# Optimization experiments

Measured on AMD Instinct MI355X. Metric: run time of the kernel, lower is better.

The kernel has to match this reference:

```python
import jax, jax.numpy as jnp
import numpy as np

N = 100_000   # nodes
E = 6_400_000  # edges (avg degree 64)
K = 3          # TAGConv hops -> K+1 linear terms per layer


def setup_inputs() -> dict:
    key = jax.random.key(0)
    ks = jax.random.split(key, 9)
    return {
        "x": jax.random.normal(ks[0], (N,), jnp.float32),
        "edge_index": jax.random.randint(ks[1], (2, E), 0, N, jnp.int32),
        "edge_attr": jax.random.normal(ks[2], (E,), jnp.float32),
        "k": 5000,
        "W1": jax.random.normal(ks[3], (K + 1, 1, 8), jnp.float32) * 0.5,
        "b1": jax.random.normal(ks[4], (8,), jnp.float32) * 0.1,
        "W2": jax.random.normal(ks[5], (K + 1, 8, 8), jnp.float32) * 0.2,
        "b2": jax.random.normal(ks[6], (8,), jnp.float32) * 0.1,
        "W3": jax.random.normal(ks[7], (K + 1, 8, 1), jnp.float32) * 0.2,
        "b3": jax.random.normal(ks[8], (1,), jnp.float32) * 0.1,
    }


def _gcn_norm(src, dst, edge_weight, num_nodes):
    # PyG gcn_norm with add_self_loops=False: deg over target index,
    # norm_e = d^{-1/2}[src] * w_e * d^{-1/2}[dst]
    deg = jax.ops.segment_sum(edge_weight, dst, num_segments=num_nodes)
    dis = jnp.where(deg > 0, jax.lax.rsqrt(jnp.where(deg > 0, deg, 1.0)), 0.0)
    return dis[src] * edge_weight * dis[dst]


def _tagconv(x, W, b, src, dst, norm, num_nodes):
    # out = sum_{h=0..K} (A_norm^h x) @ W[h] + b
    out = x @ W[0]
    h = x
    for i in range(1, W.shape[0]):
        h = jax.ops.segment_sum(norm[:, None] * h[src], dst, num_segments=num_nodes)
        out = out + h @ W[i]
    return out + b


def reference(x, edge_index, edge_attr, k, W1, b1, W2, b2, W3, b3):
    num_nodes = x.shape[0]
    x = x[:, None]  # [N, 1]
    src, dst = edge_index[0], edge_index[1]
    norm = _gcn_norm(src, dst, jnp.abs(edge_attr), num_nodes)

    x = jax.nn.relu(_tagconv(x, W1, b1, src, dst, norm, num_nodes))
    x = jax.nn.relu(_tagconv(x, W2, b2, src, dst, norm, num_nodes))
    x = jax.nn.relu(_tagconv(x, W3, b3, src, dst, norm, num_nodes))

    # tg.nn.InstanceNorm(1), batch=None, affine=False: normalize over all nodes
    mean = jnp.mean(x)
    var = jnp.mean((x - mean) ** 2)
    x = ((x - mean) * jax.lax.rsqrt(var + 1e-5)).squeeze(-1)  # [N]

    # top-k one-hot mask (argsort descending -> first k indices)
    _, top_idx = jax.lax.top_k(x, k)
    top_vec = jnp.zeros_like(x).at[top_idx].set(1.0)
    return jnp.column_stack((x, top_vec))  # [N, 2]
```

## Files before the change

kernel.cpp:

```cpp
#include <hip/hip_runtime.h>

#define BS 256
#define GPN 16
#define NBLKB 1024
#define BSH 8
#define SMAX 400

static __device__ __forceinline__ float relu_(float v) { return fmaxf(v, 0.0f); }


__global__ void k_binhist(const int* __restrict__ dst, int* __restrict__ bcnt,
                          int E, int chunk, int nbuck) {
  __shared__ int h[1024];
  int b = blockIdx.x, t = threadIdx.x;
  for (int i = t; i < nbuck; i += BS) h[i] = 0;
  __syncthreads();
  int beg = b * chunk, end = min(E, beg + chunk);
  for (int e = beg + t; e < end; e += BS) atomicAdd(&h[dst[e] >> BSH], 1);
  __syncthreads();
  for (int i = t; i < nbuck; i += BS) bcnt[(size_t)i * NBLKB + b] = h[i];
}

__global__ void k_bucketscan(int* __restrict__ bcnt, int* __restrict__ btot) {
  __shared__ int sh[BS];
  int bkt = blockIdx.x, t = threadIdx.x;
  size_t base = (size_t)bkt * NBLKB;
  int c[4], s = 0;
#pragma unroll
  for (int j = 0; j < 4; ++j) { c[j] = bcnt[base + t * 4 + j]; s += c[j]; }
  sh[t] = s; __syncthreads();
  for (int off = 1; off < BS; off <<= 1) {
    int add = (t >= off) ? sh[t - off] : 0; __syncthreads();
    sh[t] += add; __syncthreads();
  }
  int run = sh[t] - s;
#pragma unroll
  for (int j = 0; j < 4; ++j) { bcnt[base + t * 4 + j] = run; run += c[j]; }
  if (t == BS - 1) btot[bkt] = run;
}

__global__ void k_basescan(const int* __restrict__ btot, int* __restrict__ bbase, int nbuck) {
  __shared__ int sh[BS];
  int t = threadIdx.x;
  int run = 0;
  for (int c = 0; c < nbuck; c += BS) {
    int i = c + t;
    int v = (i < nbuck) ? btot[i] : 0;
    sh[t] = v; __syncthreads();
    for (int off = 1; off < BS; off <<= 1) {
      int add = (t >= off) ? sh[t - off] : 0; __syncthreads();
      sh[t] += add; __syncthreads();
    }
    if (i < nbuck) bbase[i] = run + sh[t] - v;
    run += sh[BS - 1];
    __syncthreads();
  }
}

__global__ void k_bin(const int* __restrict__ src, const int* __restrict__ dst,
                      const float* __restrict__ attr, const int* __restrict__ bcnt,
                      const int* __restrict__ bbase, int2* __restrict__ bed,
                      int E, int chunk, int nbuck) {
  __shared__ int2 stage[SMAX][8];
  __shared__ int  fc[SMAX];
  __shared__ int  cur[SMAX];
  int b = blockIdx.x, t = threadIdx.x;
  for (int i = t; i < nbuck; i += BS) {
    cur[i] = bbase[i] + bcnt[(size_t)i * NBLKB + b];
    fc[i] = 0;
  }
  __syncthreads();
  int beg = b * chunk, end = min(E, beg + chunk);
  for (int base = beg; base < end; base += BS) {
    int e = base + t;
    if (e < end) {
      int d = dst[e];
      int bkt = d >> BSH;
      int2 rec = make_int2((int)(((unsigned)(d & ((1 << BSH) - 1)) << 17) | (unsigned)src[e]),
                           __float_as_int(fabsf(attr[e])));
      int slot = atomicAdd(&fc[bkt], 1);
      if (slot < 8) stage[bkt][slot] = rec;
      else { int gp = atomicAdd(&cur[bkt], 1); bed[gp] = rec; }
    }
    __syncthreads();
    for (int i = t; i < nbuck; i += BS) {
      int c = fc[i]; if (c > 8) c = 8;
      if (c == 8) {
        int gp = cur[i]; cur[i] = gp + 8;
#pragma unroll
        for (int j = 0; j < 8; ++j) bed[gp + j] = stage[i][j];
        fc[i] = 0;
      }
    }
    __syncthreads();
  }
  for (int i = t; i < nbuck; i += BS) {
    int c = fc[i]; if (c > 8) c = 8;
    if (c) {
      int gp = cur[i];
      for (int j = 0; j < c; ++j) bed[gp + j] = stage[i][j];
    }
  }
}

__global__ void k_cntdeg(const int2* __restrict__ bed, const int* __restrict__ bbase,
                         const int* __restrict__ btot, const float* __restrict__ x,
                         float* __restrict__ dis, float* __restrict__ xhat,
                         int* __restrict__ rowptr, int N, int E) {
  __shared__ int   lc[1 << BSH];
  __shared__ float ld[1 << BSH];
  __shared__ int   sc[1 << BSH];
  int bkt = blockIdx.x, t = threadIdx.x;
  lc[t] = 0; ld[t] = 0.f;
  __syncthreads();
  int beg = bbase[bkt], tot = btot[bkt];
  for (int i = t; i < tot; i += BS) {
    int2 rec = bed[beg + i];
    int dl = (int)((unsigned)rec.x >> 17);
    atomicAdd(&lc[dl], 1);
    atomicAdd(&ld[dl], __int_as_float(rec.y));
  }
  __syncthreads();
  int c = lc[t];
  sc[t] = c;
  __syncthreads();
  for (int off = 1; off < BS; off <<= 1) {
    int add = (t >= off) ? sc[t - off] : 0; __syncthreads();
    sc[t] += add; __syncthreads();
  }
  int n = (bkt << BSH) + t;
  if (n < N) {
    rowptr[n] = beg + sc[t] - c;
    float dg = ld[t];
    float d = (dg > 0.f) ? (1.0f / sqrtf(dg)) : 0.f;
    dis[n] = d;
    xhat[n] = d * x[n];
  }
  if (t == 0 && bkt == (int)gridDim.x - 1) rowptr[N] = E;
}

__global__ void k_fill(const int2* __restrict__ bed, const int* __restrict__ bbase,
                       const int* __restrict__ btot, const int* __restrict__ rowptr,
                       int2* __restrict__ adj, int N) {
  __shared__ int2 stage[1 << BSH][8];
  __shared__ int  fc[1 << BSH];
  __shared__ int  rcur[1 << BSH];
  int bkt = blockIdx.x, t = threadIdx.x;
  int n = (bkt << BSH) + t;
  rcur[t] = (n < N) ? rowptr[n] : 0;
  fc[t] = 0;
  __syncthreads();
  int beg = bbase[bkt], tot = btot[bkt];
  for (int base = 0; base < tot; base += BS) {
    int i = base + t;
    if (i < tot) {
      int2 rec = bed[beg + i];
      unsigned u = (unsigned)rec.x;
      int dl = (int)(u >> 17);
      int2 orec = make_int2((int)(u & 0x1FFFFu), rec.y);
      int slot = atomicAdd(&fc[dl], 1);
      if (slot < 8) stage[dl][slot] = orec;
      else { int gp = atomicAdd(&rcur[dl], 1); adj[gp] = orec; }
    }
    __syncthreads();
    {
      int c = fc[t]; if (c > 8) c = 8;
      if (c == 8) {
        int gp = rcur[t]; rcur[t] = gp + 8;
#pragma unroll
        for (int j = 0; j < 8; ++j) adj[gp + j] = stage[t][j];
        fc[t] = 0;
      }
    }
    __syncthreads();
  }
  {
    int c = fc[t]; if (c > 8) c = 8;
    if (c) {
      int gp = rcur[t];
      for (int j = 0; j < c; ++j) adj[gp + j] = stage[t][j];
    }
  }
}


__global__ void k_scanA(const int* __restrict__ cnt, int* __restrict__ bsum, int N) {
  __shared__ int sh[BS];
  int t = threadIdx.x;
  int base = blockIdx.x * 1024;
  int s = 0;
#pragma unroll
  for (int j = 0; j < 4; ++j) { int i = base + t * 4 + j; s += (i < N) ? cnt[i] : 0; }
  sh[t] = s; __syncthreads();
  for (int off = 128; off; off >>= 1) { if (t < off) sh[t] += sh[t + off]; __syncthreads(); }
  if (t == 0) bsum[blockIdx.x] = sh[0];
}

__global__ void k_scanB(int* __restrict__ bsum, int NB2) {
  __shared__ int sh[BS];
  int t = threadIdx.x;
  int v = (t < NB2) ? bsum[t] : 0;
  sh[t] = v; __syncthreads();
  for (int off = 1; off < BS; off <<= 1) {
    int add = (t >= off) ? sh[t - off] : 0; __syncthreads();
    sh[t] += add; __syncthreads();
  }
  if (t < NB2) bsum[t] = sh[t] - v;
}

__global__ void k_scanC(const int* __restrict__ cnt, const int* __restrict__ bsum,
                        int* __restrict__ rowptr, int* __restrict__ cursor, int N, int E) {
  __shared__ int sh[BS];
  int b = blockIdx.x, t = threadIdx.x;
  int base = b * 1024;
  int c[4]; int s = 0;
#pragma unroll
  for (int j = 0; j < 4; ++j) { int i = base + t * 4 + j; c[j] = (i < N) ? cnt[i] : 0; s += c[j]; }
  sh[t] = s; __syncthreads();
  for (int off = 1; off < BS; off <<= 1) {
    int add = (t >= off) ? sh[t - off] : 0; __syncthreads();
    sh[t] += add; __syncthreads();
  }
  int run = sh[t] - s + bsum[b];
#pragma unroll
  for (int j = 0; j < 4; ++j) {
    int i = base + t * 4 + j;
    if (i < N) { rowptr[i] = run; if (cursor) cursor[i] = run; run += c[j]; }
  }
  if (b == 0 && t == 0) rowptr[N] = E;
}


__global__ void k_count(const int* __restrict__ dst, int* __restrict__ cnt, int E) {
  int e = blockIdx.x * blockDim.x + threadIdx.x;
  if (e < E) atomicAdd(&cnt[dst[e]], 1);
}

__global__ void k_place(const int* __restrict__ src, const int* __restrict__ dst,
                        const float* __restrict__ attr, int* __restrict__ cursor,
                        int2* __restrict__ adj, int E) {
  int e = blockIdx.x * blockDim.x + threadIdx.x;
  if (e >= E) return;
  int d = dst[e];
  int pos = atomicAdd(&cursor[d], 1);
  adj[pos] = make_int2(src[e], __float_as_int(fabsf(attr[e])));
}

__global__ void k_degdis(const int* __restrict__ rowptr, const int2* __restrict__ adj,
                         const float* __restrict__ x, float* __restrict__ dis,
                         float* __restrict__ xhat, int N) {
  int g = (blockIdx.x * blockDim.x + threadIdx.x) / GPN;
  int l = threadIdx.x & (GPN - 1);
  if (g >= N) return;
  int beg = rowptr[g], end = rowptr[g + 1];
  float s = 0.0f;
  for (int e = beg + l; e < end; e += GPN) s += __int_as_float(adj[e].y);
#pragma unroll
  for (int off = 8; off; off >>= 1) s += __shfl_xor(s, off, GPN);
  if (l == 0) {
    float d = (s > 0.0f) ? (1.0f / sqrtf(s)) : 0.0f;
    dis[g] = d;
    xhat[g] = d * x[g];
  }
}


__global__ void k_gp1_uh(const int* __restrict__ rowptr, const int2* __restrict__ adj,
                         const float* __restrict__ uin, const float* __restrict__ dis,
                         float* __restrict__ hout, float* __restrict__ uout, int N) {
  int g = (blockIdx.x * blockDim.x + threadIdx.x) / GPN;
  int l = threadIdx.x & (GPN - 1);
  if (g >= N) return;
  int beg = rowptr[g], end = rowptr[g + 1];
  float acc = 0.0f;
  for (int e = beg + l; e < end; e += GPN) {
    int2 sw = adj[e];
    acc += __int_as_float(sw.y) * uin[sw.x];
  }
#pragma unroll
  for (int off = 8; off; off >>= 1) acc += __shfl_xor(acc, off, GPN);
  if (l == 0) {
    float d = dis[g];
    float h = d * acc;
    hout[g] = h;
    uout[g] = d * h;
  }
}

__global__ void k_gp1_y(const int* __restrict__ rowptr, const int2* __restrict__ adj,
                        const float* __restrict__ u2, const float* __restrict__ x,
                        const float* __restrict__ h1, const float* __restrict__ h2,
                        const float* __restrict__ dis, const float* __restrict__ W1,
                        const float* __restrict__ b1, const float* __restrict__ W23,
                        float* __restrict__ y, float* __restrict__ Phat, int N) {
  int g = (blockIdx.x * blockDim.x + threadIdx.x) / GPN;
  int l = threadIdx.x & (GPN - 1);
  if (g >= N) return;
  int beg = rowptr[g], end = rowptr[g + 1];
  float acc = 0.0f;
  for (int e = beg + l; e < end; e += GPN) {
    int2 sw = adj[e];
    acc += __int_as_float(sw.y) * u2[sw.x];
  }
#pragma unroll
  for (int off = 8; off; off >>= 1) acc += __shfl_xor(acc, off, GPN);
  if (l == 0) {
    float d = dis[g];
    float xv = x[g], a = h1[g], b = h2[g], c = d * acc;
    float o[8];
#pragma unroll
    for (int j = 0; j < 8; ++j)
      o[j] = relu_(xv * W1[j] + a * W1[8 + j] + b * W1[16 + j] + c * W1[24 + j] + b1[j]);
    float4* op = (float4*)(y + (size_t)g * 8);
    op[0] = make_float4(o[0], o[1], o[2], o[3]);
    op[1] = make_float4(o[4], o[5], o[6], o[7]);
    float p[8];
#pragma unroll
    for (int j = 0; j < 8; ++j) {
      float s = 0.0f;
#pragma unroll
      for (int i = 0; i < 8; ++i) s += o[i] * W23[i * 8 + j];
      p[j] = d * s;
    }
    float4* pp = (float4*)(Phat + (size_t)g * 8);
    pp[0] = make_float4(p[0], p[1], p[2], p[3]);
    pp[1] = make_float4(p[4], p[5], p[6], p[7]);
  }
}

__global__ void k_gp8_u(const int* __restrict__ rowptr, const int2* __restrict__ adj,
                        const float* __restrict__ uin, const float* __restrict__ y,
                        const float* __restrict__ W, const float* __restrict__ dis,
                        float* __restrict__ uout, int N) {
  int g = (blockIdx.x * blockDim.x + threadIdx.x) / GPN;
  int l = threadIdx.x & (GPN - 1);
  if (g >= N) return;
  int beg = rowptr[g], end = rowptr[g + 1];
  float a0=0,a1=0,a2=0,a3=0,a4=0,a5=0,a6=0,a7=0;
  for (int e = beg + l; e < end; e += GPN) {
    int2 sw = adj[e];
    float w = __int_as_float(sw.y);
    const float4* hp = (const float4*)(uin + (size_t)sw.x * 8);
    float4 u = hp[0], v = hp[1];
    a0 += w*u.x; a1 += w*u.y; a2 += w*u.z; a3 += w*u.w;
    a4 += w*v.x; a5 += w*v.y; a6 += w*v.z; a7 += w*v.w;
  }
#pragma unroll
  for (int off = 8; off; off >>= 1) {
    a0 += __shfl_xor(a0, off, GPN); a1 += __shfl_xor(a1, off, GPN);
    a2 += __shfl_xor(a2, off, GPN); a3 += __shfl_xor(a3, off, GPN);
    a4 += __shfl_xor(a4, off, GPN); a5 += __shfl_xor(a5, off, GPN);
    a6 += __shfl_xor(a6, off, GPN); a7 += __shfl_xor(a7, off, GPN);
  }
  if (l == 0) {
    float d = dis[g];
    const float4* yp = (const float4*)(y + (size_t)g * 8);
    float4 u = yp[0], v = yp[1];
    float yi[8] = {u.x, u.y, u.z, u.w, v.x, v.y, v.z, v.w};
    float acc[8] = {a0, a1, a2, a3, a4, a5, a6, a7};
    float o[8];
#pragma unroll
    for (int j = 0; j < 8; ++j) {
      float s = 0.0f;
#pragma unroll
      for (int i = 0; i < 8; ++i) s += yi[i] * W[i * 8 + j];
      o[j] = d * (s + d * acc[j]);
    }
    float4* op = (float4*)(uout + (size_t)g * 8);
    op[0] = make_float4(o[0], o[1], o[2], o[3]);
    op[1] = make_float4(o[4], o[5], o[6], o[7]);
  }
}

__global__ void k_gp8_fin(const int* __restrict__ rowptr, const int2* __restrict__ adj,
                          const float* __restrict__ uin, const float* __restrict__ y,
                          const float* __restrict__ W0, const float* __restrict__ b2,
                          const float* __restrict__ W3, const float* __restrict__ dis,
                          float* __restrict__ S3hat, float* __restrict__ B2,
                          float* __restrict__ B1, float* __restrict__ B0, int N) {
  int g = (blockIdx.x * blockDim.x + threadIdx.x) / GPN;
  int l = threadIdx.x & (GPN - 1);
  if (g >= N) return;
  int beg = rowptr[g], end = rowptr[g + 1];
  float a0=0,a1=0,a2=0,a3=0,a4=0,a5=0,a6=0,a7=0;
  for (int e = beg + l; e < end; e += GPN) {
    int2 sw = adj[e];
    float w = __int_as_float(sw.y);
    const float4* hp = (const float4*)(uin + (size_t)sw.x * 8);
    float4 u = hp[0], v = hp[1];
    a0 += w*u.x; a1 += w*u.y; a2 += w*u.z; a3 += w*u.w;
    a4 += w*v.x; a5 += w*v.y; a6 += w*v.z; a7 += w*v.w;
  }
#pragma unroll
  for (int off = 8; off; off >>= 1) {
    a0 += __shfl_xor(a0, off, GPN); a1 += __shfl_xor(a1, off, GPN);
    a2 += __shfl_xor(a2, off, GPN); a3 += __shfl_xor(a3, off, GPN);
    a4 += __shfl_xor(a4, off, GPN); a5 += __shfl_xor(a5, off, GPN);
    a6 += __shfl_xor(a6, off, GPN); a7 += __shfl_xor(a7, off, GPN);
  }
  if (l == 0) {
    float d = dis[g];
    const float4* yp = (const float4*)(y + (size_t)g * 8);
    float4 u = yp[0], v = yp[1];
    float yi[8] = {u.x, u.y, u.z, u.w, v.x, v.y, v.z, v.w};
    float acc[8] = {a0, a1, a2, a3, a4, a5, a6, a7};
    float z[8];
#pragma unroll
    for (int j = 0; j < 8; ++j) {
      float s = 0.0f;
#pragma unroll
      for (int i = 0; i < 8; ++i) s += yi[i] * W0[i * 8 + j];
      z[j] = relu_(s + d * acc[j] + b2[j]);
    }
    float t[4];
#pragma unroll
    for (int i = 0; i < 4; ++i) {
      float s = 0.0f;
#pragma unroll
      for (int j = 0; j < 8; ++j) s += z[j] * W3[i * 8 + j];
      t[i] = s;
    }
    B0[g] = t[0]; B1[g] = t[1]; B2[g] = t[2];
    S3hat[g] = d * t[3];
  }
}

__global__ void k_gp1_bu(const int* __restrict__ rowptr, const int2* __restrict__ adj,
                         const float* __restrict__ uin, const float* __restrict__ B,
                         const float* __restrict__ dis, float* __restrict__ uout, int N) {
  int g = (blockIdx.x * blockDim.x + threadIdx.x) / GPN;
  int l = threadIdx.x & (GPN - 1);
  if (g >= N) return;
  int beg = rowptr[g], end = rowptr[g + 1];
  float acc = 0.0f;
  for (int e = beg + l; e < end; e += GPN) {
    int2 sw = adj[e];
    acc += __int_as_float(sw.y) * uin[sw.x];
  }
#pragma unroll
  for (int off = 8; off; off >>= 1) acc += __shfl_xor(acc, off, GPN);
  if (l == 0) {
    float d = dis[g];
    uout[g] = d * (B[g] + d * acc);
  }
}

__global__ void k_gp1_last(const int* __restrict__ rowptr, const int2* __restrict__ adj,
                           const float* __restrict__ uin, const float* __restrict__ B0,
                           const float* __restrict__ b3, const float* __restrict__ dis,
                           float* __restrict__ r, unsigned* __restrict__ keys,
                           double* __restrict__ partials, int N) {
  __shared__ double s1[BS];
  __shared__ double s2[BS];
  int tid = blockIdx.x * blockDim.x + threadIdx.x;
  int g = tid / GPN, l = tid & (GPN - 1);
  float rv = 0.0f;
  bool writer = false;
  if (g < N) {
    int beg = rowptr[g], end = rowptr[g + 1];
    float acc = 0.0f;
    for (int e = beg + l; e < end; e += GPN) {
      int2 sw = adj[e];
      acc += __int_as_float(sw.y) * uin[sw.x];
    }
#pragma unroll
    for (int off = 8; off; off >>= 1) acc += __shfl_xor(acc, off, GPN);
    if (l == 0) {
      float gg = B0[g] + dis[g] * acc;
      rv = relu_(gg + b3[0]);
      r[g] = rv;
      keys[g] = __float_as_uint(rv) | 0x80000000u;
      writer = true;
    }
  }
  double v = writer ? (double)rv : 0.0;
  s1[threadIdx.x] = v;
  s2[threadIdx.x] = v * v;
  __syncthreads();
  for (int off = 128; off; off >>= 1) {
    if (threadIdx.x < off) {
      s1[threadIdx.x] += s1[threadIdx.x + off];
      s2[threadIdx.x] += s2[threadIdx.x + off];
    }
    __syncthreads();
  }
  if (threadIdx.x == 0) {
    partials[2 * (size_t)blockIdx.x]     = s1[0];
    partials[2 * (size_t)blockIdx.x + 1] = s2[0];
  }
}

__global__ void k_stats(const double* __restrict__ partials, int nparts,
                        float* __restrict__ stats, int N) {
  __shared__ double s1[BS];
  __shared__ double s2[BS];
  int t = threadIdx.x;
  double a = 0.0, b = 0.0;
  for (int i = t; i < nparts; i += BS) { a += partials[2 * (size_t)i]; b += partials[2 * (size_t)i + 1]; }
  s1[t] = a; s2[t] = b;
  __syncthreads();
  for (int off = 128; off; off >>= 1) {
    if (t < off) { s1[t] += s1[t + off]; s2[t] += s2[t + off]; }
    __syncthreads();
  }
  if (t == 0) {
    double mean = s1[0] / (double)N;
    double var  = s2[0] / (double)N - mean * mean;
    stats[0] = (float)mean;
    stats[1] = (float)(1.0 / sqrt(var + 1e-5));
  }
}


__global__ void k_stateinit(unsigned* __restrict__ state, const int* __restrict__ kp) {
  state[0] = 0u;
  state[1] = (unsigned)kp[0];
}

__global__ void k_hist(const unsigned* __restrict__ keys, int N,
                       const unsigned* __restrict__ state, unsigned* __restrict__ hist,
                       int shift) {
  __shared__ unsigned sh[256];
  sh[threadIdx.x] = 0;
  __syncthreads();
  unsigned prefix = state[0];
  unsigned hmask = (shift >= 24) ? 0u : (0xFFFFFFFFu << (shift + 8));
  int stride = gridDim.x * blockDim.x;
  for (int n = blockIdx.x * blockDim.x + threadIdx.x; n < N; n += stride) {
    unsigned kk = keys[n];
    if ((kk & hmask) == (prefix & hmask)) atomicAdd(&sh[(kk >> shift) & 255u], 1u);
  }
  __syncthreads();
  atomicAdd(&hist[threadIdx.x], sh[threadIdx.x]);
}

__global__ void k_select(unsigned* __restrict__ state, unsigned* __restrict__ hist, int shift) {
  __shared__ unsigned sh[BS];
  int t = threadIdx.x;
  unsigned c = hist[t];
  sh[t] = c;
  __syncthreads();
  for (int off = 1; off < BS; off <<= 1) {
    unsigned add = (t + off < BS) ? sh[t + off] : 0u; __syncthreads();
    sh[t] += add; __syncthreads();
  }
  unsigned rem = state[1];
  unsigned S = sh[t];
  if (S >= rem && (S - c) < rem) {
    state[0] |= ((unsigned)t) << shift;
    state[1] = rem - (S - c);
  }
  hist[t] = 0;
}

__global__ void k_mark(const unsigned* __restrict__ keys, const float* __restrict__ r,
                       const float* __restrict__ stats, int N,
                       const unsigned* __restrict__ state, float* __restrict__ out,
                       unsigned* __restrict__ blkcnt) {
  unsigned T = state[0];
  float mean = stats[0], istd = stats[1];
  int n = blockIdx.x * 256 + threadIdx.x;
  int eq = 0;
  __shared__ int sh;
  if (threadIdx.x == 0) sh = 0;
  __syncthreads();
  if (n < N) {
    out[2 * (size_t)n] = (r[n] - mean) * istd;
    unsigned kk = keys[n];
    out[2 * (size_t)n + 1] = (kk > T) ? 1.0f : 0.0f;
    eq = (kk == T);
  }
  if (eq) atomicAdd(&sh, 1);
  __syncthreads();
  if (threadIdx.x == 0) blkcnt[blockIdx.x] = (unsigned)sh;
}

__global__ void k_scanP(const unsigned* __restrict__ blkcnt, unsigned* __restrict__ scanbuf, int NB) {
  __shared__ unsigned sh[BS];
  int t = threadIdx.x;
  unsigned c0 = (2 * t < NB) ? blkcnt[2 * t] : 0u;
  unsigned c1 = (2 * t + 1 < NB) ? blkcnt[2 * t + 1] : 0u;
  unsigned s = c0 + c1;
  sh[t] = s; __syncthreads();
  for (int off = 1; off < BS; off <<= 1) {
    unsigned add = (t >= off) ? sh[t - off] : 0u; __syncthreads();
    sh[t] += add; __syncthreads();
  }
  unsigned ex = sh[t] - s;
  if (2 * t < NB) scanbuf[2 * t] = ex;
  if (2 * t + 1 < NB) scanbuf[2 * t + 1] = ex + c0;
}

__global__ void k_resolve(const unsigned* __restrict__ keys, int N,
                          const unsigned* __restrict__ state,
                          const unsigned* __restrict__ scanbuf, float* __restrict__ out) {
  unsigned T = state[0];
  unsigned m = state[1];
  int n = blockIdx.x * 256 + threadIdx.x;
  if (n >= N) return;
  if (keys[n] != T) return;
  unsigned rank = scanbuf[blockIdx.x];
  int base = blockIdx.x * 256;
  for (int j = base; j < n; ++j) rank += (keys[j] == T);
  out[2 * (size_t)n + 1] = (rank < m) ? 1.0f : 0.0f;
}


extern "C" void kernel_launch(void* const* d_in, const int* in_sizes, int n_in,
                              void* d_out, int out_size, void* d_ws, size_t ws_size,
                              hipStream_t stream) {
  const float* x    = (const float*)d_in[0];
  const int*   ei   = (const int*)d_in[1];
  const float* attr = (const float*)d_in[2];
  const int*   kp   = (const int*)d_in[3];
  const float* W1   = (const float*)d_in[4];
  const float* b1   = (const float*)d_in[5];
  const float* W2   = (const float*)d_in[6];
  const float* b2   = (const float*)d_in[7];
  const float* W3   = (const float*)d_in[8];
  const float* b3   = (const float*)d_in[9];
  const int N = in_sizes[0];
  const int E = in_sizes[2];
  const int* src = ei;
  const int* dst = ei + E;
  float* out = (float*)d_out;
  const int NB    = (N + 255) / 256;
  const int NB2   = (N + 1023) / 1024;
  const int NBUCK = (N + (1 << BSH) - 1) >> BSH;
  const int chunk = (E + NBLKB - 1) / NBLKB;
  const int GGB   = (int)(((size_t)N * GPN + BS - 1) / BS);

  char* p = (char*)d_ws;
  auto alloc = [&](size_t bytes) -> char* {
    char* r = p; p += (bytes + 255) & ~(size_t)255; return r;
  };
  float*    dis    = (float*)alloc((size_t)N * 4);
  float*    xhat   = (float*)alloc((size_t)N * 4);
  float*    h1     = (float*)alloc((size_t)N * 4);
  float*    h2     = (float*)alloc((size_t)N * 4);
  float*    u1     = (float*)alloc((size_t)N * 4);
  float*    u2     = (float*)alloc((size_t)N * 4);
  float*    y      = (float*)alloc((size_t)N * 32);
  float*    Phat   = (float*)alloc((size_t)N * 32);
  float*    Qhat   = (float*)alloc((size_t)N * 32);
  float*    S3hat  = (float*)alloc((size_t)N * 4);
  float*    B2     = (float*)alloc((size_t)N * 4);
  float*    B1     = (float*)alloc((size_t)N * 4);
  float*    B0     = (float*)alloc((size_t)N * 4);
  float*    g2hat  = (float*)alloc((size_t)N * 4);
  float*    g1hat  = (float*)alloc((size_t)N * 4);
  float*    r      = (float*)alloc((size_t)N * 4);
  unsigned* keys   = (unsigned*)alloc((size_t)N * 4);
  double*   parts  = (double*)alloc((size_t)GGB * 16);
  float*    stats  = (float*)alloc(8);
  unsigned* state  = (unsigned*)alloc(8);
  unsigned* hist   = (unsigned*)alloc(1024);
  unsigned* blkcnt = (unsigned*)alloc((size_t)NB * 4);
  unsigned* scanbf = (unsigned*)alloc((size_t)NB * 4);
  int*      rowptr = (int*)alloc((size_t)(N + 1) * 4);
  int*      cursor = (int*)alloc((size_t)N * 4);
  int*      cnt    = (int*)alloc((size_t)N * 4);
  int*      bsum   = (int*)alloc(2048);
  int2*     adj    = (int2*)alloc((size_t)E * 8);
  size_t need_mid = (size_t)(p - (char*)d_ws);
  int2*     bed    = (int2*)alloc((size_t)E * 8);
  int*      bcnt   = (int*)alloc((size_t)NBUCK * NBLKB * 4);
  int*      btot   = (int*)alloc((size_t)NBUCK * 4 + 256);
  int*      bbase  = (int*)alloc((size_t)NBUCK * 4 + 256);
  size_t need_new = (size_t)(p - (char*)d_ws);

  dim3 B(BS);
  int genb = (E + BS - 1) / BS;
  dim3 GE(genb), GG(GGB), GN(NB), GB(NBUCK);

  bool use_new = (need_new <= ws_size) && (N <= 131072) && (NBUCK <= SMAX);

  hipMemsetAsync(hist, 0, 1024, stream);

  if (use_new) {
    k_binhist<<<dim3(NBLKB), B, 0, stream>>>(dst, bcnt, E, chunk, NBUCK);
    k_bucketscan<<<GB, B, 0, stream>>>(bcnt, btot);
    k_basescan<<<dim3(1), B, 0, stream>>>(btot, bbase, NBUCK);
    k_bin<<<dim3(NBLKB), B, 0, stream>>>(src, dst, attr, bcnt, bbase, bed, E, chunk, NBUCK);
    k_cntdeg<<<GB, B, 0, stream>>>(bed, bbase, btot, x, dis, xhat, rowptr, N, E);
    k_fill<<<GB, B, 0, stream>>>(bed, bbase, btot, rowptr, adj, N);
  } else {
    hipMemsetAsync(cnt, 0, (size_t)N * 4, stream);
    k_count<<<GE, B, 0, stream>>>(dst, cnt, E);
    k_scanA<<<dim3(NB2), B, 0, stream>>>(cnt, bsum, N);
    k_scanB<<<dim3(1), B, 0, stream>>>(bsum, NB2);
    k_scanC<<<dim3(NB2), B, 0, stream>>>(cnt, bsum, rowptr, cursor, N, E);
    k_place<<<GE, B, 0, stream>>>(src, dst, attr, cursor, adj, E);
    k_degdis<<<GG, B, 0, stream>>>(rowptr, adj, x, dis, xhat, N);
  }

  k_gp1_uh<<<GG, B, 0, stream>>>(rowptr, adj, xhat, dis, h1, u1, N);
  k_gp1_uh<<<GG, B, 0, stream>>>(rowptr, adj, u1, dis, h2, u2, N);
  k_gp1_y<<<GG, B, 0, stream>>>(rowptr, adj, u2, x, h1, h2, dis, W1, b1, W2 + 3 * 64, y, Phat, N);

  k_gp8_u<<<GG, B, 0, stream>>>(rowptr, adj, Phat, y, W2 + 2 * 64, dis, Qhat, N);
  k_gp8_u<<<GG, B, 0, stream>>>(rowptr, adj, Qhat, y, W2 + 1 * 64, dis, Phat, N);
  k_gp8_fin<<<GG, B, 0, stream>>>(rowptr, adj, Phat, y, W2, b2, W3, dis, S3hat, B2, B1, B0, N);

  k_gp1_bu<<<GG, B, 0, stream>>>(rowptr, adj, S3hat, B2, dis, g2hat, N);
  k_gp1_bu<<<GG, B, 0, stream>>>(rowptr, adj, g2hat, B1, dis, g1hat, N);
  k_gp1_last<<<GG, B, 0, stream>>>(rowptr, adj, g1hat, B0, b3, dis, r, keys, parts, N);

  k_stats<<<dim3(1), B, 0, stream>>>(parts, GGB, stats, N);

  k_stateinit<<<dim3(1), dim3(1), 0, stream>>>(state, kp);
  for (int shift = 24; shift >= 0; shift -= 8) {
    k_hist<<<GN, B, 0, stream>>>(keys, N, state, hist, shift);
    k_select<<<dim3(1), B, 0, stream>>>(state, hist, shift);
  }
  k_mark<<<GN, B, 0, stream>>>(keys, r, stats, N, state, out, blkcnt);
  k_scanP<<<dim3(1), B, 0, stream>>>(blkcnt, scanbf, NB);
  k_resolve<<<GN, B, 0, stream>>>(keys, N, state, scanbf, out);
}
```

Measured before the change: 581.9 us.

## Fuse CSR count/fill, widen binning blocks, unroll edge loops, single-block top-k select

Four separate changes. First, the degree-count and adjacency-fill kernels are merged into one 1024-thread kernel per bucket, with 16-slot staging per row. Second, the binning kernels move to 512-thread blocks, and the gather loops now use two independent accumulators per lane to expose more memory-level parallelism. Third, the four radix hist/select launch pairs are replaced by a single one-block kernel that runs all passes itself, removing launches and the global histogram memset. The cost is that this one block must serially scan all keys four times with only 256 threads.

```diff
diff --git a/kernel.cpp b/kernel.cpp
--- a/kernel.cpp
+++ b/kernel.cpp
@@ -1,6 +1,8 @@
 #include <hip/hip_runtime.h>
 
 #define BS 256
+#define BSB 512
+#define BSF 1024
 #define GPN 16
 #define NBLKB 1024
 #define BSH 8
@@ -13,12 +15,12 @@
                           int E, int chunk, int nbuck) {
   __shared__ int h[1024];
   int b = blockIdx.x, t = threadIdx.x;
-  for (int i = t; i < nbuck; i += BS) h[i] = 0;
+  for (int i = t; i < nbuck; i += BSB) h[i] = 0;
   __syncthreads();
   int beg = b * chunk, end = min(E, beg + chunk);
-  for (int e = beg + t; e < end; e += BS) atomicAdd(&h[dst[e] >> BSH], 1);
-  __syncthreads();
-  for (int i = t; i < nbuck; i += BS) bcnt[(size_t)i * NBLKB + b] = h[i];
+  for (int e = beg + t; e < end; e += BSB) atomicAdd(&h[dst[e] >> BSH], 1);
+  __syncthreads();
+  for (int i = t; i < nbuck; i += BSB) bcnt[(size_t)i * NBLKB + b] = h[i];
 }
 
 __global__ void k_bucketscan(int* __restrict__ bcnt, int* __restrict__ btot) {
@@ -65,13 +67,13 @@
   __shared__ int  fc[SMAX];
   __shared__ int  cur[SMAX];
   int b = blockIdx.x, t = threadIdx.x;
-  for (int i = t; i < nbuck; i += BS) {
+  for (int i = t; i < nbuck; i += BSB) {
     cur[i] = bbase[i] + bcnt[(size_t)i * NBLKB + b];
     fc[i] = 0;
   }
   __syncthreads();
   int beg = b * chunk, end = min(E, beg + chunk);
-  for (int base = beg; base < end; base += BS) {
+  for (int base = beg; base < end; base += BSB) {
     int e = base + t;
     if (e < end) {
       int d = dst[e];
@@ -83,7 +85,7 @@
       else { int gp = atomicAdd(&cur[bkt], 1); bed[gp] = rec; }
     }
     __syncthreads();
-    for (int i = t; i < nbuck; i += BS) {
+    for (int i = t; i < nbuck; i += BSB) {
       int c = fc[i]; if (c > 8) c = 8;
       if (c == 8) {
         int gp = cur[i]; cur[i] = gp + 8;
@@ -94,7 +96,7 @@
     }
     __syncthreads();
   }
-  for (int i = t; i < nbuck; i += BS) {
+  for (int i = t; i < nbuck; i += BSB) {
     int c = fc[i]; if (c > 8) c = 8;
     if (c) {
       int gp = cur[i];
@@ -103,55 +105,52 @@
   }
 }
 
-__global__ void k_cntdeg(const int2* __restrict__ bed, const int* __restrict__ bbase,
-                         const int* __restrict__ btot, const float* __restrict__ x,
-                         float* __restrict__ dis, float* __restrict__ xhat,
-                         int* __restrict__ rowptr, int N, int E) {
+__global__ void k_cntfill(const int2* __restrict__ bed, const int* __restrict__ bbase,
+                          const int* __restrict__ btot, const float* __restrict__ x,
+                          float* __restrict__ dis, float* __restrict__ xhat,
+                          int* __restrict__ rowptr, int2* __restrict__ adj, int N, int E) {
+  __shared__ int2  stage[1 << BSH][16];
   __shared__ int   lc[1 << BSH];
   __shared__ float ld[1 << BSH];
   __shared__ int   sc[1 << BSH];
+  __shared__ int   fc[1 << BSH];
+  __shared__ int   rcur[1 << BSH];
   int bkt = blockIdx.x, t = threadIdx.x;
-  lc[t] = 0; ld[t] = 0.f;
+  if (t < (1 << BSH)) { lc[t] = 0; ld[t] = 0.f; }
   __syncthreads();
   int beg = bbase[bkt], tot = btot[bkt];
-  for (int i = t; i < tot; i += BS) {
+  for (int i = t; i < tot; i += BSF) {
     int2 rec = bed[beg + i];
     int dl = (int)((unsigned)rec.x >> 17);
     atomicAdd(&lc[dl], 1);
     atomicAdd(&ld[dl], __int_as_float(rec.y));
   }
   __syncthreads();
-  int c = lc[t];
-  sc[t] = c;
-  __syncthreads();
-  for (int off = 1; off < BS; off <<= 1) {
-    int add = (t >= off) ? sc[t - off] : 0; __syncthreads();
-    sc[t] += add; __syncthreads();
-  }
-  int n = (bkt << BSH) + t;
-  if (n < N) {
-    rowptr[n] = beg + sc[t] - c;
-    float dg = ld[t];
-    float d = (dg > 0.f) ? (1.0f / sqrtf(dg)) : 0.f;
-    dis[n] = d;
-    xhat[n] = d * x[n];
-  }
-  if (t == 0 && bkt == (int)gridDim.x - 1) rowptr[N] = E;
-}
-
-__global__ void k_fill(const int2* __restrict__ bed, const int* __restrict__ bbase,
-                       const int* __restrict__ btot, const int* __restrict__ rowptr,
-                       int2* __restrict__ adj, int N) {
-  __shared__ int2 stage[1 << BSH][8];
-  __shared__ int  fc[1 << BSH];
-  __shared__ int  rcur[1 << BSH];
-  int bkt = blockIdx.x, t = threadIdx.x;
-  int n = (bkt << BSH) + t;
-  rcur[t] = (n < N) ? rowptr[n] : 0;
-  fc[t] = 0;
-  __syncthreads();
-  int beg = bbase[bkt], tot = btot[bkt];
-  for (int base = 0; base < tot; base += BS) {
+  if (t < (1 << BSH)) sc[t] = lc[t];
+  __syncthreads();
+  for (int off = 1; off < (1 << BSH); off <<= 1) {
+    int add = 0;
+    if (t < (1 << BSH) && t >= off) add = sc[t - off];
+    __syncthreads();
+    if (t < (1 << BSH)) sc[t] += add;
+    __syncthreads();
+  }
+  if (t < (1 << BSH)) {
+    int myrow = beg + sc[t] - lc[t];
+    rcur[t] = myrow;
+    fc[t] = 0;
+    int n = (bkt << BSH) + t;
+    if (n < N) {
+      rowptr[n] = myrow;
+      float dg = ld[t];
+      float d = (dg > 0.f) ? (1.0f / sqrtf(dg)) : 0.f;
+      dis[n] = d;
+      xhat[n] = d * x[n];
+    }
+  }
+  if (bkt == (int)gridDim.x - 1 && t == 0) rowptr[N] = E;
+  __syncthreads();
+  for (int base = 0; base < tot; base += BSF) {
     int i = base + t;
     if (i < tot) {
       int2 rec = bed[beg + i];
@@ -159,23 +158,23 @@
       int dl = (int)(u >> 17);
       int2 orec = make_int2((int)(u & 0x1FFFFu), rec.y);
       int slot = atomicAdd(&fc[dl], 1);
-      if (slot < 8) stage[dl][slot] = orec;
+      if (slot < 16) stage[dl][slot] = orec;
       else { int gp = atomicAdd(&rcur[dl], 1); adj[gp] = orec; }
     }
     __syncthreads();
-    {
-      int c = fc[t]; if (c > 8) c = 8;
-      if (c == 8) {
-        int gp = rcur[t]; rcur[t] = gp + 8;
-#pragma unroll
-        for (int j = 0; j < 8; ++j) adj[gp + j] = stage[t][j];
+    if (t < (1 << BSH)) {
+      int c = fc[t]; if (c > 16) c = 16;
+      if (c == 16) {
+        int gp = rcur[t]; rcur[t] = gp + 16;
+#pragma unroll
+        for (int j = 0; j < 16; ++j) adj[gp + j] = stage[t][j];
         fc[t] = 0;
       }
     }
     __syncthreads();
   }
-  {
-    int c = fc[t]; if (c > 8) c = 8;
+  if (t < (1 << BSH)) {
+    int c = fc[t]; if (c > 16) c = 16;
     if (c) {
       int gp = rcur[t];
       for (int j = 0; j < c; ++j) adj[gp + j] = stage[t][j];
@@ -229,7 +228,6 @@
   }
   if (b == 0 && t == 0) rowptr[N] = E;
 }
-
 
 __global__ void k_count(const int* __restrict__ dst, int* __restrict__ cnt, int E) {
   int e = blockIdx.x * blockDim.x + threadIdx.x;
@@ -265,20 +263,31 @@
 }
 
 
+static __device__ __forceinline__ float edge_sum1(const int2* __restrict__ adj,
+                                                  const float* __restrict__ uin,
+                                                  int beg, int end, int l) {
+  float acc0 = 0.0f, acc1 = 0.0f;
+  int e = beg + l;
+  int last = end - GPN;
+  for (; e < last; e += 2 * GPN) {
+    int2 s0 = adj[e], s1 = adj[e + GPN];
+    acc0 += __int_as_float(s0.y) * uin[s0.x];
+    acc1 += __int_as_float(s1.y) * uin[s1.x];
+  }
+  if (e < end) { int2 s0 = adj[e]; acc0 += __int_as_float(s0.y) * uin[s0.x]; }
+  float acc = acc0 + acc1;
+#pragma unroll
+  for (int off = 8; off; off >>= 1) acc += __shfl_xor(acc, off, GPN);
+  return acc;
+}
+
 __global__ void k_gp1_uh(const int* __restrict__ rowptr, const int2* __restrict__ adj,
                          const float* __restrict__ uin, const float* __restrict__ dis,
                          float* __restrict__ hout, float* __restrict__ uout, int N) {
   int g = (blockIdx.x * blockDim.x + threadIdx.x) / GPN;
   int l = threadIdx.x & (GPN - 1);
   if (g >= N) return;
-  int beg = rowptr[g], end = rowptr[g + 1];
-  float acc = 0.0f;
-  for (int e = beg + l; e < end; e += GPN) {
-    int2 sw = adj[e];
-    acc += __int_as_float(sw.y) * uin[sw.x];
-  }
-#pragma unroll
-  for (int off = 8; off; off >>= 1) acc += __shfl_xor(acc, off, GPN);
+  float acc = edge_sum1(adj, uin, rowptr[g], rowptr[g + 1], l);
   if (l == 0) {
     float d = dis[g];
     float h = d * acc;
@@ -296,14 +305,7 @@
   int g = (blockIdx.x * blockDim.x + threadIdx.x) / GPN;
   int l = threadIdx.x & (GPN - 1);
   if (g >= N) return;
-  int beg = rowptr[g], end = rowptr[g + 1];
-  float acc = 0.0f;
-  for (int e = beg + l; e < end; e += GPN) {
-    int2 sw = adj[e];
-    acc += __int_as_float(sw.y) * u2[sw.x];
-  }
-#pragma unroll
-  for (int off = 8; off; off >>= 1) acc += __shfl_xor(acc, off, GPN);
+  float acc = edge_sum1(adj, u2, rowptr[g], rowptr[g + 1], l);
   if (l == 0) {
     float d = dis[g];
     float xv = x[g], a = h1[g], b = h2[g], c = d * acc;
@@ -327,6 +329,39 @@
     pp[1] = make_float4(p[4], p[5], p[6], p[7]);
   }
 }
+
+#define EDGE_SUM8(ADJ, UIN, BEG, END, L)                                        \
+  float a0=0,a1=0,a2=0,a3=0,a4=0,a5=0,a6=0,a7=0;                                \
+  {                                                                             \
+    int e = (BEG) + (L);                                                        \
+    int last = (END) - GPN;                                                     \
+    for (; e < last; e += 2 * GPN) {                                            \
+      int2 s0 = (ADJ)[e], s1 = (ADJ)[e + GPN];                                  \
+      float w0 = __int_as_float(s0.y), w1 = __int_as_float(s1.y);               \
+      const float4* p0 = (const float4*)((UIN) + (size_t)s0.x * 8);             \
+      const float4* p1 = (const float4*)((UIN) + (size_t)s1.x * 8);             \
+      float4 u0 = p0[0], v0 = p0[1], u1 = p1[0], v1 = p1[1];                    \
+      a0 += w0*u0.x; a1 += w0*u0.y; a2 += w0*u0.z; a3 += w0*u0.w;               \
+      a4 += w0*v0.x; a5 += w0*v0.y; a6 += w0*v0.z; a7 += w0*v0.w;               \
+      a0 += w1*u1.x; a1 += w1*u1.y; a2 += w1*u1.z; a3 += w1*u1.w;               \
+      a4 += w1*v1.x; a5 += w1*v1.y; a6 += w1*v1.z; a7 += w1*v1.w;               \
+    }                                                                           \
+    if (e < (END)) {                                                            \
+      int2 s0 = (ADJ)[e];                                                       \
+      float w0 = __int_as_float(s0.y);                                          \
+      const float4* p0 = (const float4*)((UIN) + (size_t)s0.x * 8);             \
+      float4 u0 = p0[0], v0 = p0[1];                                            \
+      a0 += w0*u0.x; a1 += w0*u0.y; a2 += w0*u0.z; a3 += w0*u0.w;               \
+      a4 += w0*v0.x; a5 += w0*v0.y; a6 += w0*v0.z; a7 += w0*v0.w;               \
+    }                                                                           \
+  }                                                                             \
+  _Pragma("unroll")                                                             \
+  for (int off = 8; off; off >>= 1) {                                           \
+    a0 += __shfl_xor(a0, off, GPN); a1 += __shfl_xor(a1, off, GPN);             \
+    a2 += __shfl_xor(a2, off, GPN); a3 += __shfl_xor(a3, off, GPN);             \
+    a4 += __shfl_xor(a4, off, GPN); a5 += __shfl_xor(a5, off, GPN);             \
+    a6 += __shfl_xor(a6, off, GPN); a7 += __shfl_xor(a7, off, GPN);             \
+  }
 
 __global__ void k_gp8_u(const int* __restrict__ rowptr, const int2* __restrict__ adj,
                         const float* __restrict__ uin, const float* __restrict__ y,
@@ -336,22 +371,7 @@
   int l = threadIdx.x & (GPN - 1);
   if (g >= N) return;
   int beg = rowptr[g], end = rowptr[g + 1];
-  float a0=0,a1=0,a2=0,a3=0,a4=0,a5=0,a6=0,a7=0;
-  for (int e = beg + l; e < end; e += GPN) {
-    int2 sw = adj[e];
-    float w = __int_as_float(sw.y);
-    const float4* hp = (const float4*)(uin + (size_t)sw.x * 8);
-    float4 u = hp[0], v = hp[1];
-    a0 += w*u.x; a1 += w*u.y; a2 += w*u.z; a3 += w*u.w;
-    a4 += w*v.x; a5 += w*v.y; a6 += w*v.z; a7 += w*v.w;
-  }
-#pragma unroll
-  for (int off = 8; off; off >>= 1) {
-    a0 += __shfl_xor(a0, off, GPN); a1 += __shfl_xor(a1, off, GPN);
-    a2 += __shfl_xor(a2, off, GPN); a3 += __shfl_xor(a3, off, GPN);
-    a4 += __shfl_xor(a4, off, GPN); a5 += __shfl_xor(a5, off, GPN);
-    a6 += __shfl_xor(a6, off, GPN); a7 += __shfl_xor(a7, off, GPN);
-  }
+  EDGE_SUM8(adj, uin, beg, end, l)
   if (l == 0) {
     float d = dis[g];
     const float4* yp = (const float4*)(y + (size_t)g * 8);
@@ -382,22 +402,7 @@
   int l = threadIdx.x & (GPN - 1);
   if (g >= N) return;
   int beg = rowptr[g], end = rowptr[g + 1];
-  float a0=0,a1=0,a2=0,a3=0,a4=0,a5=0,a6=0,a7=0;
-  for (int e = beg + l; e < end; e += GPN) {
-    int2 sw = adj[e];
-    float w = __int_as_float(sw.y);
-    const float4* hp = (const float4*)(uin + (size_t)sw.x * 8);
-    float4 u = hp[0], v = hp[1];
-    a0 += w*u.x; a1 += w*u.y; a2 += w*u.z; a3 += w*u.w;
-    a4 += w*v.x; a5 += w*v.y; a6 += w*v.z; a7 += w*v.w;
-  }
-#pragma unroll
-  for (int off = 8; off; off >>= 1) {
-    a0 += __shfl_xor(a0, off, GPN); a1 += __shfl_xor(a1, off, GPN);
-    a2 += __shfl_xor(a2, off, GPN); a3 += __shfl_xor(a3, off, GPN);
-    a4 += __shfl_xor(a4, off, GPN); a5 += __shfl_xor(a5, off, GPN);
-    a6 += __shfl_xor(a6, off, GPN); a7 += __shfl_xor(a7, off, GPN);
-  }
+  EDGE_SUM8(adj, uin, beg, end, l)
   if (l == 0) {
     float d = dis[g];
     const float4* yp = (const float4*)(y + (size_t)g * 8);
@@ -412,16 +417,16 @@
       for (int i = 0; i < 8; ++i) s += yi[i] * W0[i * 8 + j];
       z[j] = relu_(s + d * acc[j] + b2[j]);
     }
-    float t[4];
+    float tt[4];
 #pragma unroll
     for (int i = 0; i < 4; ++i) {
       float s = 0.0f;
 #pragma unroll
       for (int j = 0; j < 8; ++j) s += z[j] * W3[i * 8 + j];
-      t[i] = s;
-    }
-    B0[g] = t[0]; B1[g] = t[1]; B2[g] = t[2];
-    S3hat[g] = d * t[3];
+      tt[i] = s;
+    }
+    B0[g] = tt[0]; B1[g] = tt[1]; B2[g] = tt[2];
+    S3hat[g] = d * tt[3];
   }
 }
 
@@ -431,14 +436,7 @@
   int g = (blockIdx.x * blockDim.x + threadIdx.x) / GPN;
   int l = threadIdx.x & (GPN - 1);
   if (g >= N) return;
-  int beg = rowptr[g], end = rowptr[g + 1];
-  float acc = 0.0f;
-  for (int e = beg + l; e < end; e += GPN) {
-    int2 sw = adj[e];
-    acc += __int_as_float(sw.y) * uin[sw.x];
-  }
-#pragma unroll
-  for (int off = 8; off; off >>= 1) acc += __shfl_xor(acc, off, GPN);
+  float acc = edge_sum1(adj, uin, rowptr[g], rowptr[g + 1], l);
   if (l == 0) {
     float d = dis[g];
     uout[g] = d * (B[g] + d * acc);
@@ -457,14 +455,7 @@
   float rv = 0.0f;
   bool writer = false;
   if (g < N) {
-    int beg = rowptr[g], end = rowptr[g + 1];
-    float acc = 0.0f;
-    for (int e = beg + l; e < end; e += GPN) {
-      int2 sw = adj[e];
-      acc += __int_as_float(sw.y) * uin[sw.x];
-    }
-#pragma unroll
-    for (int off = 8; off; off >>= 1) acc += __shfl_xor(acc, off, GPN);
+    float acc = edge_sum1(adj, uin, rowptr[g], rowptr[g + 1], l);
     if (l == 0) {
       float gg = B0[g] + dis[g] * acc;
       rv = relu_(gg + b3[0]);
@@ -512,45 +503,39 @@
 }
 
 
-__global__ void k_stateinit(unsigned* __restrict__ state, const int* __restrict__ kp) {
-  state[0] = 0u;
-  state[1] = (unsigned)kp[0];
-}
-
-__global__ void k_hist(const unsigned* __restrict__ keys, int N,
-                       const unsigned* __restrict__ state, unsigned* __restrict__ hist,
-                       int shift) {
-  __shared__ unsigned sh[256];
-  sh[threadIdx.x] = 0;
-  __syncthreads();
-  unsigned prefix = state[0];
-  unsigned hmask = (shift >= 24) ? 0u : (0xFFFFFFFFu << (shift + 8));
-  int stride = gridDim.x * blockDim.x;
-  for (int n = blockIdx.x * blockDim.x + threadIdx.x; n < N; n += stride) {
-    unsigned kk = keys[n];
-    if ((kk & hmask) == (prefix & hmask)) atomicAdd(&sh[(kk >> shift) & 255u], 1u);
-  }
-  __syncthreads();
-  atomicAdd(&hist[threadIdx.x], sh[threadIdx.x]);
-}
-
-__global__ void k_select(unsigned* __restrict__ state, unsigned* __restrict__ hist, int shift) {
-  __shared__ unsigned sh[BS];
+__global__ void k_topksel(const unsigned* __restrict__ keys, int N,
+                          const int* __restrict__ kp, unsigned* __restrict__ state) {
+  __shared__ unsigned hist[256];
+  __shared__ unsigned sfx[256];
+  __shared__ unsigned s_pick, s_rem;
   int t = threadIdx.x;
-  unsigned c = hist[t];
-  sh[t] = c;
-  __syncthreads();
-  for (int off = 1; off < BS; off <<= 1) {
-    unsigned add = (t + off < BS) ? sh[t + off] : 0u; __syncthreads();
-    sh[t] += add; __syncthreads();
-  }
-  unsigned rem = state[1];
-  unsigned S = sh[t];
-  if (S >= rem && (S - c) < rem) {
-    state[0] |= ((unsigned)t) << shift;
-    state[1] = rem - (S - c);
-  }
-  hist[t] = 0;
+  unsigned prefix = 0;
+  unsigned rem = (unsigned)kp[0];
+  for (int shift = 24; shift >= 0; shift -= 8) {
+    hist[t] = 0;
+    __syncthreads();
+    unsigned hmask = (shift >= 24) ? 0u : (0xFFFFFFFFu << (shift + 8));
+    for (int n = t; n < N; n += 256) {
+      unsigned kk = keys[n];
+      if ((kk & hmask) == (prefix & hmask)) atomicAdd(&hist[(kk >> shift) & 255u], 1u);
+    }
+    __syncthreads();
+    sfx[t] = hist[t];
+    __syncthreads();
+    for (int off = 1; off < 256; off <<= 1) {
+      unsigned add = (t + off < 256) ? sfx[t + off] : 0u;
+      __syncthreads();
+      sfx[t] += add;
+      __syncthreads();
+    }
+    unsigned S = sfx[t], c = hist[t];
+    if (S >= rem && (S - c) < rem) { s_pick = (unsigned)t; s_rem = rem - (S - c); }
+    __syncthreads();
+    prefix |= s_pick << shift;
+    rem = s_rem;
+    __syncthreads();
+  }
+  if (t == 0) { state[0] = prefix; state[1] = rem; }
 }
 
 __global__ void k_mark(const unsigned* __restrict__ keys, const float* __restrict__ r,
@@ -654,7 +639,6 @@
   double*   parts  = (double*)alloc((size_t)GGB * 16);
   float*    stats  = (float*)alloc(8);
   unsigned* state  = (unsigned*)alloc(8);
-  unsigned* hist   = (unsigned*)alloc(1024);
   unsigned* blkcnt = (unsigned*)alloc((size_t)NB * 4);
   unsigned* scanbf = (unsigned*)alloc((size_t)NB * 4);
   int*      rowptr = (int*)alloc((size_t)(N + 1) * 4);
@@ -662,7 +646,6 @@
   int*      cnt    = (int*)alloc((size_t)N * 4);
   int*      bsum   = (int*)alloc(2048);
   int2*     adj    = (int2*)alloc((size_t)E * 8);
-  size_t need_mid = (size_t)(p - (char*)d_ws);
   int2*     bed    = (int2*)alloc((size_t)E * 8);
   int*      bcnt   = (int*)alloc((size_t)NBUCK * NBLKB * 4);
   int*      btot   = (int*)alloc((size_t)NBUCK * 4 + 256);
@@ -673,17 +656,14 @@
   int genb = (E + BS - 1) / BS;
   dim3 GE(genb), GG(GGB), GN(NB), GB(NBUCK);
 
-  bool use_new = (need_new <= ws_size) && (N <= 131072) && (NBUCK <= SMAX);
-
-  hipMemsetAsync(hist, 0, 1024, stream);
+  bool use_new = (need_new <= ws_size) && (N <= 102400) && (NBUCK <= SMAX);
 
   if (use_new) {
-    k_binhist<<<dim3(NBLKB), B, 0, stream>>>(dst, bcnt, E, chunk, NBUCK);
+    k_binhist<<<dim3(NBLKB), dim3(BSB), 0, stream>>>(dst, bcnt, E, chunk, NBUCK);
     k_bucketscan<<<GB, B, 0, stream>>>(bcnt, btot);
     k_basescan<<<dim3(1), B, 0, stream>>>(btot, bbase, NBUCK);
-    k_bin<<<dim3(NBLKB), B, 0, stream>>>(src, dst, attr, bcnt, bbase, bed, E, chunk, NBUCK);
-    k_cntdeg<<<GB, B, 0, stream>>>(bed, bbase, btot, x, dis, xhat, rowptr, N, E);
-    k_fill<<<GB, B, 0, stream>>>(bed, bbase, btot, rowptr, adj, N);
+    k_bin<<<dim3(NBLKB), dim3(BSB), 0, stream>>>(src, dst, attr, bcnt, bbase, bed, E, chunk, NBUCK);
+    k_cntfill<<<GB, dim3(BSF), 0, stream>>>(bed, bbase, btot, x, dis, xhat, rowptr, adj, N, E);
   } else {
     hipMemsetAsync(cnt, 0, (size_t)N * 4, stream);
     k_count<<<GE, B, 0, stream>>>(dst, cnt, E);
@@ -708,11 +688,7 @@
 
   k_stats<<<dim3(1), B, 0, stream>>>(parts, GGB, stats, N);
 
-  k_stateinit<<<dim3(1), dim3(1), 0, stream>>>(state, kp);
-  for (int shift = 24; shift >= 0; shift -= 8) {
-    k_hist<<<GN, B, 0, stream>>>(keys, N, state, hist, shift);
-    k_select<<<dim3(1), B, 0, stream>>>(state, hist, shift);
-  }
+  k_topksel<<<dim3(1), B, 0, stream>>>(keys, N, kp, state);
   k_mark<<<GN, B, 0, stream>>>(keys, r, stats, N, state, out, blkcnt);
   k_scanP<<<dim3(1), B, 0, stream>>>(blkcnt, scanbf, NB);
   k_resolve<<<GN, B, 0, stream>>>(keys, N, state, scanbf, out);
```

Result: slower. 831.9 us (+43.0%).
